# Performance work log

Measured on AMD Instinct MI355X. Metric: run time of the kernel, lower is better.

## Reference

```python
import jax, jax.numpy as jnp
import numpy as np

NUM_CODES = 1296
D_DIM = 64


def setup_inputs() -> dict:
    key = jax.random.key(0)
    k1, k2 = jax.random.split(key)
    inputs = jax.random.normal(k1, (32, 64, 64, D_DIM), dtype=jnp.float32)
    # lecun_normal init: stddev = 1/sqrt(fan_in) with fan_in = d
    embeddings = jax.random.normal(k2, (NUM_CODES, D_DIM), dtype=jnp.float32) / np.sqrt(D_DIM)
    return {"inputs": inputs, "embeddings": embeddings}


def reference(inputs, embeddings):
    x1 = jnp.sum(inputs ** 2, axis=-1, keepdims=True)          # [b,m,n,1]
    x2 = jnp.sum(embeddings ** 2, axis=-1)                      # [k]
    x3 = jnp.einsum('bmnd,kd->bmnk', inputs, embeddings)        # [b,m,n,k]
    D = x1 + x2 - 2.0 * x3
    codes = jnp.argmin(D, axis=-1).astype(jnp.int32)            # [b,m,n]
    code_vecs = embeddings[codes]                               # [b,m,n,d]
    return codes, code_vecs
```

## Files before the change

kernel.cpp:

```cpp
#include <hip/hip_runtime.h>

#define NUM_CODES 1296
#define PAD_CODES 1344
#define DDIM 64
#define NUM_Q 131072
#define THREADS 256
#define QPW 32
#define QPB 128
#define MARGIN 0.25f
#define SLOTS 24
#define CHUNK 96
#define NSTEP 14

typedef __attribute__((ext_vector_type(8))) short bf16x8;
typedef __attribute__((ext_vector_type(4))) float f32x4;

__device__ __forceinline__ ushort f2bf(float f) {
    unsigned u = __float_as_uint(f);
    return (ushort)((u + 0x7fffu + ((u >> 16) & 1u)) >> 16);
}

__global__ __launch_bounds__(64) void vq_prep(const float* __restrict__ emb,
                                              float* __restrict__ enorm,
                                              ushort* __restrict__ eh) {
    int k = blockIdx.x * 64 + threadIdx.x;
    if (k >= PAD_CODES) return;
    int ks = k < NUM_CODES ? k : NUM_CODES - 1;
    const float* e = emb + (size_t)ks * DDIM;
    float f[DDIM];
#pragma unroll
    for (int i = 0; i < 16; ++i) {
        float4 v = *(const float4*)(e + 4 * i);
        f[4*i] = v.x; f[4*i+1] = v.y; f[4*i+2] = v.z; f[4*i+3] = v.w;
    }
    {
#pragma clang fp contract(off)
        float r8[8];
#pragma unroll
        for (int j = 0; j < 8; ++j) { float t = f[j] * f[j]; r8[j] = t; }
#pragma unroll
        for (int i = 1; i < 8; ++i) {
#pragma unroll
            for (int j = 0; j < 8; ++j) { float t = f[i*8+j] * f[i*8+j]; r8[j] += t; }
        }
        enorm[k] = ((r8[0]+r8[1])+(r8[2]+r8[3])) + ((r8[4]+r8[5])+(r8[6]+r8[7]));
    }
    ushort h[DDIM];
#pragma unroll
    for (int d = 0; d < DDIM; ++d) h[d] = f2bf(f[d]);
    uint* dh = (uint*)(eh + (size_t)k * DDIM);
#pragma unroll
    for (int s = 0; s < 8; ++s) {
        int ds = s ^ (k & 7);
#pragma unroll
        for (int j = 0; j < 4; ++j)
            dh[ds*4 + j] = (uint)h[s*8 + 2*j] | ((uint)h[s*8 + 2*j + 1] << 16);
    }
}

__global__ __launch_bounds__(256) void vq_xnorm(const float* __restrict__ x,
                                                float* __restrict__ xnorm) {
    int q = blockIdx.x * 256 + threadIdx.x;
    const float* r = x + (size_t)q * DDIM;
    float f[DDIM];
#pragma unroll
    for (int i = 0; i < 16; ++i) {
        float4 v = *(const float4*)(r + 4 * i);
        f[4*i] = v.x; f[4*i+1] = v.y; f[4*i+2] = v.z; f[4*i+3] = v.w;
    }
    {
#pragma clang fp contract(off)
        float r8[8];
#pragma unroll
        for (int j = 0; j < 8; ++j) { float t = f[j] * f[j]; r8[j] = t; }
#pragma unroll
        for (int i = 1; i < 8; ++i) {
#pragma unroll
            for (int j = 0; j < 8; ++j) { float t = f[i*8+j] * f[i*8+j]; r8[j] += t; }
        }
        xnorm[q] = ((r8[0]+r8[1])+(r8[2]+r8[3])) + ((r8[4]+r8[5])+(r8[6]+r8[7]));
    }
}

__global__ __launch_bounds__(THREADS) void vq_main(
        const float* __restrict__ x, const float* __restrict__ emb,
        const float* __restrict__ enorm_g, const float* __restrict__ xnorm,
        const ushort* __restrict__ eh, float* __restrict__ out) {
    __shared__ ushort sbuf[2][CHUNK * DDIM];
    __shared__ float sen[PAD_CODES];
    __shared__ ushort wq[4][QPW * SLOTS];
    __shared__ unsigned qcnt[4][QPW];
    __shared__ unsigned skk[4][QPW];

    const int tid  = threadIdx.x;
    const int lane = tid & 63;
    const int w    = tid >> 6;
    const int cl   = lane & 15;
    const int g    = lane >> 4;
    const long qw  = (long)blockIdx.x * QPB + w * QPW;

    if (lane < QPW) qcnt[w][lane] = 0;

    bf16x8 a00, a01, a10, a11;
    {
        const float* xp0 = x + (qw + cl) * DDIM + g * 8;
        const float* xp1 = xp0 + 16 * DDIM;
#pragma unroll
        for (int j = 0; j < 8; ++j) {
            a00[j] = (short)f2bf(xp0[j]);
            a01[j] = (short)f2bf(xp0[j + 32]);
            a10[j] = (short)f2bf(xp1[j]);
            a11[j] = (short)f2bf(xp1[j + 32]);
        }
    }

    float rmin0[4], rmin1[4];
#pragma unroll
    for (int r = 0; r < 4; ++r) { rmin0[r] = __builtin_inff(); rmin1[r] = __builtin_inff(); }

    const int slot0 = (g     ^ (cl & 7)) * 8;
    const int slot1 = ((g+4) ^ (cl & 7)) * 8;
    const f32x4 z4 = {0.f, 0.f, 0.f, 0.f};

    {
        const float4* src = (const float4*)eh;
        float4 s0 = src[tid], s1 = src[256 + tid], s2 = src[512 + tid];
        *(float4*)&sbuf[0][(size_t)tid * 8]         = s0;
        *(float4*)&sbuf[0][(size_t)(256 + tid) * 8] = s1;
        *(float4*)&sbuf[0][(size_t)(512 + tid) * 8] = s2;
        for (int i = tid; i < PAD_CODES; i += THREADS) sen[i] = enorm_g[i];
    }
    __syncthreads();

#define MFMA_TILE(T, D0, D1) { \
        const ushort* bp_ = &sbuf[cur][(size_t)((T) * 16 + cl) * DDIM]; \
        bf16x8 b0_ = *(const bf16x8*)(bp_ + slot0); \
        bf16x8 b1_ = *(const bf16x8*)(bp_ + slot1); \
        D0 = __builtin_amdgcn_mfma_f32_16x16x32_bf16(a00, b0_, z4, 0, 0, 0); \
        D1 = __builtin_amdgcn_mfma_f32_16x16x32_bf16(a10, b0_, z4, 0, 0, 0); \
        D0 = __builtin_amdgcn_mfma_f32_16x16x32_bf16(a01, b1_, D0, 0, 0, 0); \
        D1 = __builtin_amdgcn_mfma_f32_16x16x32_bf16(a11, b1_, D1, 0, 0, 0); }

#define SCORE_TILE(T, D0, D1) { \
        float en_ = sen[cb + (T) * 16 + cl]; \
        _Pragma("unroll") \
        for (int r = 0; r < 4; ++r) { \
            D0[r] = fmaf(-2.f, D0[r], en_); \
            D1[r] = fmaf(-2.f, D1[r], en_); \
            rmin0[r] = fminf(rmin0[r], D0[r]); \
            rmin1[r] = fminf(rmin1[r], D1[r]); } }

#define TEST_TILE(T, D0, D1) { \
        const int c_ = cb + (T) * 16 + cl; \
        if (c_ < NUM_CODES) { \
            _Pragma("unroll") \
            for (int r = 0; r < 4; ++r) { \
                if (D0[r] <= thr0[r]) { \
                    unsigned i_ = atomicAdd(&qcnt[w][g*4 + r], 1u); \
                    if (i_ < SLOTS) wq[w][(g*4 + r) * SLOTS + i_] = (ushort)c_; } \
                if (D1[r] <= thr1[r]) { \
                    unsigned i_ = atomicAdd(&qcnt[w][16 + g*4 + r], 1u); \
                    if (i_ < SLOTS) wq[w][(16 + g*4 + r) * SLOTS + i_] = (ushort)c_; } } } }

    int cur = 0;
    for (int s = 0; s < NSTEP; ++s) {
        float4 n0, n1, n2;
        const bool more = (s + 1 < NSTEP);
        if (more) {
            const float4* src = (const float4*)(eh + (size_t)(s + 1) * CHUNK * DDIM);
            n0 = src[tid]; n1 = src[256 + tid]; n2 = src[512 + tid];
        }
        const int cb = s * CHUNK;
        f32x4 d00, d01, d02, d03, d04, d05;
        f32x4 d10, d11, d12, d13, d14, d15;
        MFMA_TILE(0, d00, d10); MFMA_TILE(1, d01, d11); MFMA_TILE(2, d02, d12);
        MFMA_TILE(3, d03, d13); MFMA_TILE(4, d04, d14); MFMA_TILE(5, d05, d15);
        SCORE_TILE(0, d00, d10); SCORE_TILE(1, d01, d11); SCORE_TILE(2, d02, d12);
        SCORE_TILE(3, d03, d13); SCORE_TILE(4, d04, d14); SCORE_TILE(5, d05, d15);
#pragma unroll
        for (int m = 1; m < 16; m <<= 1) {
#pragma unroll
            for (int r = 0; r < 4; ++r) {
                rmin0[r] = fminf(rmin0[r], __shfl_xor(rmin0[r], m, 64));
                rmin1[r] = fminf(rmin1[r], __shfl_xor(rmin1[r], m, 64));
            }
        }
        float thr0[4], thr1[4];
#pragma unroll
        for (int r = 0; r < 4; ++r) { thr0[r] = rmin0[r] + MARGIN; thr1[r] = rmin1[r] + MARGIN; }
        if (more) {
            *(float4*)&sbuf[cur ^ 1][(size_t)tid * 8]         = n0;
            *(float4*)&sbuf[cur ^ 1][(size_t)(256 + tid) * 8] = n1;
            *(float4*)&sbuf[cur ^ 1][(size_t)(512 + tid) * 8] = n2;
        }
        __syncthreads();
        TEST_TILE(0, d00, d10); TEST_TILE(1, d01, d11); TEST_TILE(2, d02, d12);
        TEST_TILE(3, d03, d13); TEST_TILE(4, d04, d14); TEST_TILE(5, d05, d15);
        cur ^= 1;
    }

    auto exact_pk = [&](int c, long gq) -> unsigned long long {
        const float* xr = x + gq * DDIM;
        const float* er = emb + (size_t)c * DDIM;
        float dot = 0.f;
#pragma unroll
        for (int p4 = 0; p4 < 16; ++p4) {
            float4 xv = *(const float4*)(xr + 4 * p4);
            float4 ev = *(const float4*)(er + 4 * p4);
            dot = fmaf(xv.x, ev.x, dot); dot = fmaf(xv.y, ev.y, dot);
            dot = fmaf(xv.z, ev.z, dot); dot = fmaf(xv.w, ev.w, dot);
        }
        float dist = (xnorm[gq] + sen[c]) - 2.f * dot;
        unsigned u = __float_as_uint(dist);
        unsigned key = (u & 0x80000000u) ? ~u : (u | 0x80000000u);
        return ((unsigned long long)key << 32) | (unsigned)c;
    };

    const int grp = lane >> 3, gl = lane & 7;
#pragma unroll
    for (int qo = 0; qo < 4; ++qo) {
        const int ql = qo * 8 + grp;
        const long gq = qw + ql;
        const unsigned nq = qcnt[w][ql];
        unsigned long long pk = ~0ULL;
        if (nq <= SLOTS) {
            for (unsigned i = gl; i < nq; i += 8) {
                unsigned long long t = exact_pk((int)wq[w][ql * SLOTS + i], gq);
                if (t < pk) pk = t;
            }
        }
#pragma unroll
        for (int m = 1; m < 8; m <<= 1) {
            unsigned long long o = (unsigned long long)__shfl_xor((long long)pk, m, 64);
            if (o < pk) pk = o;
        }
        if (gl == 0 && nq <= SLOTS) {
            skk[w][ql] = (unsigned)pk;
            out[gq] = (float)(unsigned)pk;
        }
    }
    for (int ql = 0; ql < QPW; ++ql) {
        if (qcnt[w][ql] <= SLOTS) continue;
        const long gq = qw + ql;
        unsigned long long pk = ~0ULL;
        for (int t = 0; t < 21; ++t) {
            int c = lane + (t << 6);
            if (c < NUM_CODES) {
                unsigned long long tp = exact_pk(c, gq);
                if (tp < pk) pk = tp;
            }
        }
#pragma unroll
        for (int m = 1; m < 64; m <<= 1) {
            unsigned long long o = (unsigned long long)__shfl_xor((long long)pk, m, 64);
            if (o < pk) pk = o;
        }
        if (lane == 0) {
            skk[w][ql] = (unsigned)pk;
            out[gq] = (float)(unsigned)pk;
        }
    }

    const int gu = lane >> 4, gv = lane & 15;
#pragma unroll
    for (int qo = 0; qo < 8; ++qo) {
        const int ql = qo * 4 + gu;
        const unsigned kk = skk[w][ql];
        const long gq = qw + ql;
        *(float4*)(out + (long)NUM_Q + gq * DDIM + gv * 4) =
            *(const float4*)(emb + (size_t)kk * DDIM + gv * 4);
    }
}

extern "C" void kernel_launch(void* const* d_in, const int* in_sizes, int n_in,
                              void* d_out, int out_size, void* d_ws, size_t ws_size,
                              hipStream_t stream) {
    const float* x   = (const float*)d_in[0];
    const float* emb = (const float*)d_in[1];
    float*  enorm = (float*)d_ws;
    float*  xnorm = (float*)((char*)d_ws + 8192);
    ushort* eh    = (ushort*)((char*)d_ws + 532480);

    hipLaunchKernelGGL(vq_prep, dim3(PAD_CODES / 64), dim3(64), 0, stream,
                       emb, enorm, eh);
    hipLaunchKernelGGL(vq_xnorm, dim3(NUM_Q / 256), dim3(256), 0, stream,
                       x, xnorm);
    hipLaunchKernelGGL(vq_main, dim3(NUM_Q / QPB), dim3(THREADS), 0, stream,
                       x, emb, enorm, xnorm, eh, (float*)d_out);
}
```

Baseline: 129.8 us.

## Process two query sets per wave to reuse codebook fragments

```diff
diff --git a/kernel.cpp b/kernel.cpp
--- a/kernel.cpp
+++ b/kernel.cpp
@@ -5,10 +5,10 @@
 #define DDIM 64
 #define NUM_Q 131072
 #define THREADS 256
-#define QPW 32
-#define QPB 128
+#define QPW 64
+#define QPB 256
 #define MARGIN 0.25f
-#define SLOTS 24
+#define SLOTS 16
 #define CHUNK 96
 #define NSTEP 14
 
@@ -99,24 +99,29 @@
     const int g    = lane >> 4;
     const long qw  = (long)blockIdx.x * QPB + w * QPW;
 
-    if (lane < QPW) qcnt[w][lane] = 0;
-
-    bf16x8 a00, a01, a10, a11;
+    for (int i = lane; i < QPW; i += 64) qcnt[w][i] = 0;
+
+    bf16x8 A0_00, A0_01, A0_10, A0_11, A1_00, A1_01, A1_10, A1_11;
     {
-        const float* xp0 = x + (qw + cl) * DDIM + g * 8;
-        const float* xp1 = xp0 + 16 * DDIM;
+        const float* p0 = x + (qw + cl) * DDIM + g * 8;
+        const float* p1 = p0 + 16 * DDIM;
+        const float* p2 = p0 + 32 * DDIM;
+        const float* p3 = p0 + 48 * DDIM;
 #pragma unroll
         for (int j = 0; j < 8; ++j) {
-            a00[j] = (short)f2bf(xp0[j]);
-            a01[j] = (short)f2bf(xp0[j + 32]);
-            a10[j] = (short)f2bf(xp1[j]);
-            a11[j] = (short)f2bf(xp1[j + 32]);
-        }
-    }
-
-    float rmin0[4], rmin1[4];
-#pragma unroll
-    for (int r = 0; r < 4; ++r) { rmin0[r] = __builtin_inff(); rmin1[r] = __builtin_inff(); }
+            A0_00[j] = (short)f2bf(p0[j]); A0_01[j] = (short)f2bf(p0[j + 32]);
+            A0_10[j] = (short)f2bf(p1[j]); A0_11[j] = (short)f2bf(p1[j + 32]);
+            A1_00[j] = (short)f2bf(p2[j]); A1_01[j] = (short)f2bf(p2[j + 32]);
+            A1_10[j] = (short)f2bf(p3[j]); A1_11[j] = (short)f2bf(p3[j + 32]);
+        }
+    }
+
+    float rm0s0[4], rm1s0[4], rm0s1[4], rm1s1[4];
+#pragma unroll
+    for (int r = 0; r < 4; ++r) {
+        rm0s0[r] = __builtin_inff(); rm1s0[r] = __builtin_inff();
+        rm0s1[r] = __builtin_inff(); rm1s1[r] = __builtin_inff();
+    }
 
     const int slot0 = (g     ^ (cl & 7)) * 8;
     const int slot1 = ((g+4) ^ (cl & 7)) * 8;
@@ -132,35 +137,59 @@
     }
     __syncthreads();
 
-#define MFMA_TILE(T, D0, D1) { \
+#define MFMA_TILE(T, AL0, AL1, AH0, AH1, D0, D1) { \
         const ushort* bp_ = &sbuf[cur][(size_t)((T) * 16 + cl) * DDIM]; \
         bf16x8 b0_ = *(const bf16x8*)(bp_ + slot0); \
         bf16x8 b1_ = *(const bf16x8*)(bp_ + slot1); \
-        D0 = __builtin_amdgcn_mfma_f32_16x16x32_bf16(a00, b0_, z4, 0, 0, 0); \
-        D1 = __builtin_amdgcn_mfma_f32_16x16x32_bf16(a10, b0_, z4, 0, 0, 0); \
-        D0 = __builtin_amdgcn_mfma_f32_16x16x32_bf16(a01, b1_, D0, 0, 0, 0); \
-        D1 = __builtin_amdgcn_mfma_f32_16x16x32_bf16(a11, b1_, D1, 0, 0, 0); }
-
-#define SCORE_TILE(T, D0, D1) { \
+        D0 = __builtin_amdgcn_mfma_f32_16x16x32_bf16(AL0, b0_, z4, 0, 0, 0); \
+        D1 = __builtin_amdgcn_mfma_f32_16x16x32_bf16(AH0, b0_, z4, 0, 0, 0); \
+        D0 = __builtin_amdgcn_mfma_f32_16x16x32_bf16(AL1, b1_, D0, 0, 0, 0); \
+        D1 = __builtin_amdgcn_mfma_f32_16x16x32_bf16(AH1, b1_, D1, 0, 0, 0); }
+
+#define SCORE_TILE(T, D0, D1, RM0, RM1) { \
         float en_ = sen[cb + (T) * 16 + cl]; \
         _Pragma("unroll") \
         for (int r = 0; r < 4; ++r) { \
             D0[r] = fmaf(-2.f, D0[r], en_); \
             D1[r] = fmaf(-2.f, D1[r], en_); \
-            rmin0[r] = fminf(rmin0[r], D0[r]); \
-            rmin1[r] = fminf(rmin1[r], D1[r]); } }
-
-#define TEST_TILE(T, D0, D1) { \
+            RM0[r] = fminf(RM0[r], D0[r]); \
+            RM1[r] = fminf(RM1[r], D1[r]); } }
+
+#define TEST_TILE(T, D0, D1, QB) { \
         const int c_ = cb + (T) * 16 + cl; \
         if (c_ < NUM_CODES) { \
             _Pragma("unroll") \
             for (int r = 0; r < 4; ++r) { \
                 if (D0[r] <= thr0[r]) { \
-                    unsigned i_ = atomicAdd(&qcnt[w][g*4 + r], 1u); \
-                    if (i_ < SLOTS) wq[w][(g*4 + r) * SLOTS + i_] = (ushort)c_; } \
+                    unsigned i_ = atomicAdd(&qcnt[w][(QB) + g*4 + r], 1u); \
+                    if (i_ < SLOTS) wq[w][((QB) + g*4 + r) * SLOTS + i_] = (ushort)c_; } \
                 if (D1[r] <= thr1[r]) { \
-                    unsigned i_ = atomicAdd(&qcnt[w][16 + g*4 + r], 1u); \
-                    if (i_ < SLOTS) wq[w][(16 + g*4 + r) * SLOTS + i_] = (ushort)c_; } } } }
+                    unsigned i_ = atomicAdd(&qcnt[w][(QB) + 16 + g*4 + r], 1u); \
+                    if (i_ < SLOTS) wq[w][((QB) + 16 + g*4 + r) * SLOTS + i_] = (ushort)c_; } } } }
+
+#define DO_SET(AL0, AL1, AH0, AH1, RM0, RM1, QB) { \
+        f32x4 d00, d01, d02, d03, d04, d05, d10, d11, d12, d13, d14, d15; \
+        MFMA_TILE(0, AL0, AL1, AH0, AH1, d00, d10); \
+        MFMA_TILE(1, AL0, AL1, AH0, AH1, d01, d11); \
+        MFMA_TILE(2, AL0, AL1, AH0, AH1, d02, d12); \
+        MFMA_TILE(3, AL0, AL1, AH0, AH1, d03, d13); \
+        MFMA_TILE(4, AL0, AL1, AH0, AH1, d04, d14); \
+        MFMA_TILE(5, AL0, AL1, AH0, AH1, d05, d15); \
+        SCORE_TILE(0, d00, d10, RM0, RM1); SCORE_TILE(1, d01, d11, RM0, RM1); \
+        SCORE_TILE(2, d02, d12, RM0, RM1); SCORE_TILE(3, d03, d13, RM0, RM1); \
+        SCORE_TILE(4, d04, d14, RM0, RM1); SCORE_TILE(5, d05, d15, RM0, RM1); \
+        _Pragma("unroll") \
+        for (int m = 1; m < 16; m <<= 1) { \
+            _Pragma("unroll") \
+            for (int r = 0; r < 4; ++r) { \
+                RM0[r] = fminf(RM0[r], __shfl_xor(RM0[r], m, 64)); \
+                RM1[r] = fminf(RM1[r], __shfl_xor(RM1[r], m, 64)); } } \
+        float thr0[4], thr1[4]; \
+        _Pragma("unroll") \
+        for (int r = 0; r < 4; ++r) { thr0[r] = RM0[r] + MARGIN; thr1[r] = RM1[r] + MARGIN; } \
+        TEST_TILE(0, d00, d10, QB); TEST_TILE(1, d01, d11, QB); \
+        TEST_TILE(2, d02, d12, QB); TEST_TILE(3, d03, d13, QB); \
+        TEST_TILE(4, d04, d14, QB); TEST_TILE(5, d05, d15, QB); }
 
     int cur = 0;
     for (int s = 0; s < NSTEP; ++s) {
@@ -171,31 +200,14 @@
             n0 = src[tid]; n1 = src[256 + tid]; n2 = src[512 + tid];
         }
         const int cb = s * CHUNK;
-        f32x4 d00, d01, d02, d03, d04, d05;
-        f32x4 d10, d11, d12, d13, d14, d15;
-        MFMA_TILE(0, d00, d10); MFMA_TILE(1, d01, d11); MFMA_TILE(2, d02, d12);
-        MFMA_TILE(3, d03, d13); MFMA_TILE(4, d04, d14); MFMA_TILE(5, d05, d15);
-        SCORE_TILE(0, d00, d10); SCORE_TILE(1, d01, d11); SCORE_TILE(2, d02, d12);
-        SCORE_TILE(3, d03, d13); SCORE_TILE(4, d04, d14); SCORE_TILE(5, d05, d15);
-#pragma unroll
-        for (int m = 1; m < 16; m <<= 1) {
-#pragma unroll
-            for (int r = 0; r < 4; ++r) {
-                rmin0[r] = fminf(rmin0[r], __shfl_xor(rmin0[r], m, 64));
-                rmin1[r] = fminf(rmin1[r], __shfl_xor(rmin1[r], m, 64));
-            }
-        }
-        float thr0[4], thr1[4];
-#pragma unroll
-        for (int r = 0; r < 4; ++r) { thr0[r] = rmin0[r] + MARGIN; thr1[r] = rmin1[r] + MARGIN; }
+        DO_SET(A0_00, A0_01, A0_10, A0_11, rm0s0, rm1s0, 0);
+        DO_SET(A1_00, A1_01, A1_10, A1_11, rm0s1, rm1s1, 32);
         if (more) {
             *(float4*)&sbuf[cur ^ 1][(size_t)tid * 8]         = n0;
             *(float4*)&sbuf[cur ^ 1][(size_t)(256 + tid) * 8] = n1;
             *(float4*)&sbuf[cur ^ 1][(size_t)(512 + tid) * 8] = n2;
         }
         __syncthreads();
-        TEST_TILE(0, d00, d10); TEST_TILE(1, d01, d11); TEST_TILE(2, d02, d12);
-        TEST_TILE(3, d03, d13); TEST_TILE(4, d04, d14); TEST_TILE(5, d05, d15);
         cur ^= 1;
     }
 
@@ -218,7 +230,7 @@
 
     const int grp = lane >> 3, gl = lane & 7;
 #pragma unroll
-    for (int qo = 0; qo < 4; ++qo) {
+    for (int qo = 0; qo < 8; ++qo) {
         const int ql = qo * 8 + grp;
         const long gq = qw + ql;
         const unsigned nq = qcnt[w][ql];
@@ -263,7 +275,7 @@
 
     const int gu = lane >> 4, gv = lane & 15;
 #pragma unroll
-    for (int qo = 0; qo < 8; ++qo) {
+    for (int qo = 0; qo < 16; ++qo) {
         const int ql = qo * 4 + gu;
         const unsigned kk = skk[w][ql];
         const long gq = qw + ql;
```

After: 212.7 us. 63.9% more time.

## Fuse x-norm kernel into main kernel via shared-memory staged query tile

Applied to the files above, without the earlier changes.

```diff
diff --git a/kernel.cpp b/kernel.cpp
--- a/kernel.cpp
+++ b/kernel.cpp
@@ -8,9 +8,10 @@
 #define QPW 32
 #define QPB 128
 #define MARGIN 0.25f
-#define SLOTS 24
+#define SLOTS 16
 #define CHUNK 96
 #define NSTEP 14
+#define SXP 68
 
 typedef __attribute__((ext_vector_type(8))) short bf16x8;
 typedef __attribute__((ext_vector_type(4))) float f32x4;
@@ -58,36 +59,14 @@
     }
 }
 
-__global__ __launch_bounds__(256) void vq_xnorm(const float* __restrict__ x,
-                                                float* __restrict__ xnorm) {
-    int q = blockIdx.x * 256 + threadIdx.x;
-    const float* r = x + (size_t)q * DDIM;
-    float f[DDIM];
-#pragma unroll
-    for (int i = 0; i < 16; ++i) {
-        float4 v = *(const float4*)(r + 4 * i);
-        f[4*i] = v.x; f[4*i+1] = v.y; f[4*i+2] = v.z; f[4*i+3] = v.w;
-    }
-    {
-#pragma clang fp contract(off)
-        float r8[8];
-#pragma unroll
-        for (int j = 0; j < 8; ++j) { float t = f[j] * f[j]; r8[j] = t; }
-#pragma unroll
-        for (int i = 1; i < 8; ++i) {
-#pragma unroll
-            for (int j = 0; j < 8; ++j) { float t = f[i*8+j] * f[i*8+j]; r8[j] += t; }
-        }
-        xnorm[q] = ((r8[0]+r8[1])+(r8[2]+r8[3])) + ((r8[4]+r8[5])+(r8[6]+r8[7]));
-    }
-}
-
 __global__ __launch_bounds__(THREADS) void vq_main(
         const float* __restrict__ x, const float* __restrict__ emb,
-        const float* __restrict__ enorm_g, const float* __restrict__ xnorm,
-        const ushort* __restrict__ eh, float* __restrict__ out) {
+        const float* __restrict__ enorm_g, const ushort* __restrict__ eh,
+        float* __restrict__ out) {
     __shared__ ushort sbuf[2][CHUNK * DDIM];
+    __shared__ float sx[QPB * SXP];
     __shared__ float sen[PAD_CODES];
+    __shared__ float x1s[QPB];
     __shared__ ushort wq[4][QPW * SLOTS];
     __shared__ unsigned qcnt[4][QPW];
     __shared__ unsigned skk[4][QPW];
@@ -98,31 +77,18 @@
     const int cl   = lane & 15;
     const int g    = lane >> 4;
     const long qw  = (long)blockIdx.x * QPB + w * QPW;
+    const int qloc0 = w * QPW;
 
     if (lane < QPW) qcnt[w][lane] = 0;
 
-    bf16x8 a00, a01, a10, a11;
     {
-        const float* xp0 = x + (qw + cl) * DDIM + g * 8;
-        const float* xp1 = xp0 + 16 * DDIM;
-#pragma unroll
-        for (int j = 0; j < 8; ++j) {
-            a00[j] = (short)f2bf(xp0[j]);
-            a01[j] = (short)f2bf(xp0[j + 32]);
-            a10[j] = (short)f2bf(xp1[j]);
-            a11[j] = (short)f2bf(xp1[j + 32]);
-        }
-    }
-
-    float rmin0[4], rmin1[4];
-#pragma unroll
-    for (int r = 0; r < 4; ++r) { rmin0[r] = __builtin_inff(); rmin1[r] = __builtin_inff(); }
-
-    const int slot0 = (g     ^ (cl & 7)) * 8;
-    const int slot1 = ((g+4) ^ (cl & 7)) * 8;
-    const f32x4 z4 = {0.f, 0.f, 0.f, 0.f};
-
-    {
+        const float4* xsrc = (const float4*)(x + (size_t)blockIdx.x * QPB * DDIM);
+#pragma unroll
+        for (int u = 0; u < 8; ++u) {
+            int idx = u * THREADS + tid;
+            int r = idx >> 4, j = idx & 15;
+            *(float4*)&sx[r * SXP + j * 4] = xsrc[idx];
+        }
         const float4* src = (const float4*)eh;
         float4 s0 = src[tid], s1 = src[256 + tid], s2 = src[512 + tid];
         *(float4*)&sbuf[0][(size_t)tid * 8]         = s0;
@@ -131,6 +97,40 @@
         for (int i = tid; i < PAD_CODES; i += THREADS) sen[i] = enorm_g[i];
     }
     __syncthreads();
+
+    if (tid < QPB) {
+#pragma clang fp contract(off)
+        float r8[8];
+#pragma unroll
+        for (int j = 0; j < 8; ++j) { float v = sx[tid*SXP + j]; float t = v*v; r8[j] = t; }
+#pragma unroll
+        for (int i = 1; i < 8; ++i) {
+#pragma unroll
+            for (int j = 0; j < 8; ++j) { float v = sx[tid*SXP + i*8 + j]; float t = v*v; r8[j] += t; }
+        }
+        x1s[tid] = ((r8[0]+r8[1])+(r8[2]+r8[3])) + ((r8[4]+r8[5])+(r8[6]+r8[7]));
+    }
+
+    bf16x8 a00, a01, a10, a11;
+    {
+        const float* xr0 = &sx[(qloc0 + cl) * SXP + g * 8];
+        const float* xr1 = xr0 + 16 * SXP;
+#pragma unroll
+        for (int j = 0; j < 8; ++j) {
+            a00[j] = (short)f2bf(xr0[j]);
+            a01[j] = (short)f2bf(xr0[j + 32]);
+            a10[j] = (short)f2bf(xr1[j]);
+            a11[j] = (short)f2bf(xr1[j + 32]);
+        }
+    }
+
+    float rmin0[4], rmin1[4];
+#pragma unroll
+    for (int r = 0; r < 4; ++r) { rmin0[r] = __builtin_inff(); rmin1[r] = __builtin_inff(); }
+
+    const int slot0 = (g     ^ (cl & 7)) * 8;
+    const int slot1 = ((g+4) ^ (cl & 7)) * 8;
+    const f32x4 z4 = {0.f, 0.f, 0.f, 0.f};
 
 #define MFMA_TILE(T, D0, D1) { \
         const ushort* bp_ = &sbuf[cur][(size_t)((T) * 16 + cl) * DDIM]; \
@@ -199,8 +199,8 @@
         cur ^= 1;
     }
 
-    auto exact_pk = [&](int c, long gq) -> unsigned long long {
-        const float* xr = x + gq * DDIM;
+    auto exact_pk = [&](int c, int qloc) -> unsigned long long {
+        const float* xr = &sx[qloc * SXP];
         const float* er = emb + (size_t)c * DDIM;
         float dot = 0.f;
 #pragma unroll
@@ -210,7 +210,7 @@
             dot = fmaf(xv.x, ev.x, dot); dot = fmaf(xv.y, ev.y, dot);
             dot = fmaf(xv.z, ev.z, dot); dot = fmaf(xv.w, ev.w, dot);
         }
-        float dist = (xnorm[gq] + sen[c]) - 2.f * dot;
+        float dist = (x1s[qloc] + sen[c]) - 2.f * dot;
         unsigned u = __float_as_uint(dist);
         unsigned key = (u & 0x80000000u) ? ~u : (u | 0x80000000u);
         return ((unsigned long long)key << 32) | (unsigned)c;
@@ -220,12 +220,11 @@
 #pragma unroll
     for (int qo = 0; qo < 4; ++qo) {
         const int ql = qo * 8 + grp;
-        const long gq = qw + ql;
         const unsigned nq = qcnt[w][ql];
         unsigned long long pk = ~0ULL;
         if (nq <= SLOTS) {
             for (unsigned i = gl; i < nq; i += 8) {
-                unsigned long long t = exact_pk((int)wq[w][ql * SLOTS + i], gq);
+                unsigned long long t = exact_pk((int)wq[w][ql * SLOTS + i], qloc0 + ql);
                 if (t < pk) pk = t;
             }
         }
@@ -236,17 +235,16 @@
         }
         if (gl == 0 && nq <= SLOTS) {
             skk[w][ql] = (unsigned)pk;
-            out[gq] = (float)(unsigned)pk;
+            out[qw + ql] = (float)(unsigned)pk;
         }
     }
     for (int ql = 0; ql < QPW; ++ql) {
         if (qcnt[w][ql] <= SLOTS) continue;
-        const long gq = qw + ql;
         unsigned long long pk = ~0ULL;
         for (int t = 0; t < 21; ++t) {
             int c = lane + (t << 6);
             if (c < NUM_CODES) {
-                unsigned long long tp = exact_pk(c, gq);
+                unsigned long long tp = exact_pk(c, qloc0 + ql);
                 if (tp < pk) pk = tp;
             }
         }
@@ -257,7 +255,7 @@
         }
         if (lane == 0) {
             skk[w][ql] = (unsigned)pk;
-            out[gq] = (float)(unsigned)pk;
+            out[qw + ql] = (float)(unsigned)pk;
         }
     }
 
@@ -278,13 +276,10 @@
     const float* x   = (const float*)d_in[0];
     const float* emb = (const float*)d_in[1];
     float*  enorm = (float*)d_ws;
-    float*  xnorm = (float*)((char*)d_ws + 8192);
-    ushort* eh    = (ushort*)((char*)d_ws + 532480);
+    ushort* eh    = (ushort*)((char*)d_ws + 8192);
 
     hipLaunchKernelGGL(vq_prep, dim3(PAD_CODES / 64), dim3(64), 0, stream,
                        emb, enorm, eh);
-    hipLaunchKernelGGL(vq_xnorm, dim3(NUM_Q / 256), dim3(256), 0, stream,
-                       x, xnorm);
     hipLaunchKernelGGL(vq_main, dim3(NUM_Q / QPB), dim3(THREADS), 0, stream,
-                       x, emb, enorm, xnorm, eh, (float*)d_out);
-}
+                       x, emb, enorm, eh, (float*)d_out);
+}
```

Measured after the change: 127.9 us, median of 2. Within noise of the previous version (-1.5%).

## Load codebook chunks via direct global-to-LDS, shrink blocks, use DPP reductions

Applied to the files above, without the earlier changes.

```diff
diff --git a/kernel.cpp b/kernel.cpp
--- a/kernel.cpp
+++ b/kernel.cpp
@@ -4,11 +4,12 @@
 #define PAD_CODES 1344
 #define DDIM 64
 #define NUM_Q 131072
-#define THREADS 256
+#define THREADS 128
+#define WAVES 2
 #define QPW 32
-#define QPB 128
+#define QPB 64
 #define MARGIN 0.25f
-#define SLOTS 24
+#define SLOTS 16
 #define CHUNK 96
 #define NSTEP 14
 
@@ -19,6 +20,17 @@
     unsigned u = __float_as_uint(f);
     return (ushort)((u + 0x7fffu + ((u >> 16) & 1u)) >> 16);
 }
+
+__device__ __forceinline__ void gl_lds(const ushort* g, ushort* l) {
+    __builtin_amdgcn_global_load_lds(
+        (const __attribute__((address_space(1))) unsigned int*)(g),
+        (__attribute__((address_space(3))) unsigned int*)(l), 16, 0, 0);
+}
+
+#define DPPMIN(v, ctrl) { \
+    int t_ = __builtin_amdgcn_update_dpp(0, __float_as_int(v), ctrl, 0xf, 0xf, true); \
+    v = fminf(v, __int_as_float(t_)); }
+#define DPPRED16(v) { DPPMIN(v, 0xB1) DPPMIN(v, 0x4E) DPPMIN(v, 0x141) DPPMIN(v, 0x140) }
 
 __global__ __launch_bounds__(64) void vq_prep(const float* __restrict__ emb,
                                               float* __restrict__ enorm,
@@ -87,10 +99,9 @@
         const float* __restrict__ enorm_g, const float* __restrict__ xnorm,
         const ushort* __restrict__ eh, float* __restrict__ out) {
     __shared__ ushort sbuf[2][CHUNK * DDIM];
-    __shared__ float sen[PAD_CODES];
-    __shared__ ushort wq[4][QPW * SLOTS];
-    __shared__ unsigned qcnt[4][QPW];
-    __shared__ unsigned skk[4][QPW];
+    __shared__ ushort wq[WAVES][QPW * SLOTS];
+    __shared__ unsigned qcnt[WAVES][QPW];
+    __shared__ unsigned skk[WAVES][QPW];
 
     const int tid  = threadIdx.x;
     const int lane = tid & 63;
@@ -123,12 +134,10 @@
     const f32x4 z4 = {0.f, 0.f, 0.f, 0.f};
 
     {
-        const float4* src = (const float4*)eh;
-        float4 s0 = src[tid], s1 = src[256 + tid], s2 = src[512 + tid];
-        *(float4*)&sbuf[0][(size_t)tid * 8]         = s0;
-        *(float4*)&sbuf[0][(size_t)(256 + tid) * 8] = s1;
-        *(float4*)&sbuf[0][(size_t)(512 + tid) * 8] = s2;
-        for (int i = tid; i < PAD_CODES; i += THREADS) sen[i] = enorm_g[i];
+#pragma unroll
+        for (int k = 0; k < 6; ++k)
+            gl_lds(eh + (size_t)(k * THREADS + tid) * 8,
+                   &sbuf[0][(size_t)(k * THREADS + tid) * 8]);
     }
     __syncthreads();
 
@@ -142,7 +151,7 @@
         D1 = __builtin_amdgcn_mfma_f32_16x16x32_bf16(a11, b1_, D1, 0, 0, 0); }
 
 #define SCORE_TILE(T, D0, D1) { \
-        float en_ = sen[cb + (T) * 16 + cl]; \
+        float en_ = en[T]; \
         _Pragma("unroll") \
         for (int r = 0; r < 4; ++r) { \
             D0[r] = fmaf(-2.f, D0[r], en_); \
@@ -164,13 +173,19 @@
 
     int cur = 0;
     for (int s = 0; s < NSTEP; ++s) {
-        float4 n0, n1, n2;
         const bool more = (s + 1 < NSTEP);
         if (more) {
-            const float4* src = (const float4*)(eh + (size_t)(s + 1) * CHUNK * DDIM);
-            n0 = src[tid]; n1 = src[256 + tid]; n2 = src[512 + tid];
+            const ushort* src = eh + (size_t)(s + 1) * CHUNK * DDIM;
+#pragma unroll
+            for (int k = 0; k < 6; ++k)
+                gl_lds(src + (size_t)(k * THREADS + tid) * 8,
+                       &sbuf[cur ^ 1][(size_t)(k * THREADS + tid) * 8]);
         }
         const int cb = s * CHUNK;
+        float en[6];
+#pragma unroll
+        for (int t = 0; t < 6; ++t) en[t] = enorm_g[cb + t * 16 + cl];
+
         f32x4 d00, d01, d02, d03, d04, d05;
         f32x4 d10, d11, d12, d13, d14, d15;
         MFMA_TILE(0, d00, d10); MFMA_TILE(1, d01, d11); MFMA_TILE(2, d02, d12);
@@ -178,21 +193,10 @@
         SCORE_TILE(0, d00, d10); SCORE_TILE(1, d01, d11); SCORE_TILE(2, d02, d12);
         SCORE_TILE(3, d03, d13); SCORE_TILE(4, d04, d14); SCORE_TILE(5, d05, d15);
 #pragma unroll
-        for (int m = 1; m < 16; m <<= 1) {
-#pragma unroll
-            for (int r = 0; r < 4; ++r) {
-                rmin0[r] = fminf(rmin0[r], __shfl_xor(rmin0[r], m, 64));
-                rmin1[r] = fminf(rmin1[r], __shfl_xor(rmin1[r], m, 64));
-            }
-        }
+        for (int r = 0; r < 4; ++r) { DPPRED16(rmin0[r]); DPPRED16(rmin1[r]); }
         float thr0[4], thr1[4];
 #pragma unroll
         for (int r = 0; r < 4; ++r) { thr0[r] = rmin0[r] + MARGIN; thr1[r] = rmin1[r] + MARGIN; }
-        if (more) {
-            *(float4*)&sbuf[cur ^ 1][(size_t)tid * 8]         = n0;
-            *(float4*)&sbuf[cur ^ 1][(size_t)(256 + tid) * 8] = n1;
-            *(float4*)&sbuf[cur ^ 1][(size_t)(512 + tid) * 8] = n2;
-        }
         __syncthreads();
         TEST_TILE(0, d00, d10); TEST_TILE(1, d01, d11); TEST_TILE(2, d02, d12);
         TEST_TILE(3, d03, d13); TEST_TILE(4, d04, d14); TEST_TILE(5, d05, d15);
@@ -210,7 +214,7 @@
             dot = fmaf(xv.x, ev.x, dot); dot = fmaf(xv.y, ev.y, dot);
             dot = fmaf(xv.z, ev.z, dot); dot = fmaf(xv.w, ev.w, dot);
         }
-        float dist = (xnorm[gq] + sen[c]) - 2.f * dot;
+        float dist = (xnorm[gq] + enorm_g[c]) - 2.f * dot;
         unsigned u = __float_as_uint(dist);
         unsigned key = (u & 0x80000000u) ? ~u : (u | 0x80000000u);
         return ((unsigned long long)key << 32) | (unsigned)c;
```

Result: slower. 152.7 us (+17.7%).
